# Kernel tuning notes

Measured on AMD Instinct MI355X. Metric: run time of the kernel, lower is better.

The kernel has to match this reference:

```python
import jax, jax.numpy as jnp
import numpy as np

Q_R = jnp.array([-1.0 / np.sqrt(2.0), 1.0 / np.sqrt(2.0)], dtype=jnp.float32)
N_U, N_H, N_MLP, N_CONV, N_Q = 8, 12, 16, 2, 2


def setup_inputs() -> dict:
    B, n = 16, 1024
    key = jax.random.key(0)
    ks = jax.random.split(key, 24)
    lin_w = lambda k, o, i: (jax.random.normal(k, (o, i), jnp.float32) * 0.1)
    lin_b = lambda k, o: (jax.random.normal(k, (o,), jnp.float32) * 0.1)
    inp = {
        "y": jax.random.normal(ks[0], (B, n), jnp.float32),
        "H": jax.random.normal(ks[1], (B, n, n), jnp.float32),
        "r": jax.random.normal(ks[2], (B, n), jnp.float32),
        "nu_r": jax.random.uniform(ks[3], (B, n), jnp.float32),
        "adj": (jax.random.uniform(ks[4], (B, n, n)) < 0.05).astype(jnp.float32),
        # W1: Linear(2, n_u) plus extra bias b1
        "W1_w": lin_w(ks[5], N_U, 2), "W1_b": lin_b(ks[6], N_U),
        "b1": jnp.zeros((N_U,), jnp.float32),
        # msg_mlp: Linear(3*n_u, n_mlp_hidden) -> ReLU -> Linear(n_mlp_hidden, n_u)
        "Wm1_w": lin_w(ks[7], N_MLP, 3 * N_U), "Wm1_b": lin_b(ks[8], N_MLP),
        "Wm2_w": lin_w(ks[9], N_U, N_MLP), "Wm2_b": lin_b(ks[10], N_U),
        # GRUCell(n_u + 2, n_h); gate order: r, z, n
        "gru_w_ih": lin_w(ks[11], 3 * N_H, N_U + 2), "gru_w_hh": lin_w(ks[12], 3 * N_H, N_H),
        "gru_b_ih": lin_b(ks[13], 3 * N_H), "gru_b_hh": lin_b(ks[14], 3 * N_H),
        # W2: Linear(n_h, n_u) plus extra bias b2
        "W2_w": lin_w(ks[15], N_U, N_H), "W2_b": lin_b(ks[16], N_U),
        "b2": jnp.zeros((N_U,), jnp.float32),
        # readout: Linear(n_u, n_mlp_hidden) -> ReLU -> Linear(n_mlp_hidden, N_Q)
        "Wr1_w": lin_w(ks[17], N_MLP, N_U), "Wr1_b": lin_b(ks[18], N_MLP),
        "Wr2_w": lin_w(ks[19], N_Q, N_MLP), "Wr2_b": lin_b(ks[20], N_Q),
    }
    return inp


def reference(y, H, r, nu_r, adj, W1_w, W1_b, b1, Wm1_w, Wm1_b, Wm2_w, Wm2_b,
              gru_w_ih, gru_w_hh, gru_b_ih, gru_b_hh, W2_w, W2_b, b2,
              Wr1_w, Wr1_b, Wr2_w, Wr2_b):
    B, n = y.shape
    yh = jnp.einsum('bi,bij->bj', y, H)          # (B,n)
    hh = jnp.sum(H * H, axis=1)                  # (B,n), column norms
    feat = jnp.stack([yh, hh], axis=-1)          # (B,n,2)
    u = feat @ W1_w.T + W1_b + b1                # (B,n,n_u)
    G = jnp.einsum('bki,bkj->bij', H, H)         # H^T H, (B,n,n)
    a_i = jnp.stack([r, jnp.maximum(nu_r, 1e-10)], axis=-1)  # (B,n,2)

    # masked-sum aggregation, fused (same math as expand+cat+mask+sum):
    #   agg = [u_i * deg_i, sum_j adj_ij u_j, (sum_j adj_ij G_ij) * 1_{n_u}]
    deg = jnp.sum(adj, axis=2)                   # (B,n)
    eg = jnp.sum(adj * G, axis=2)                # (B,n)
    eg_part = jnp.repeat(eg[..., None], N_U, axis=-1)  # (B,n,n_u)

    s = jnp.zeros((B, n, N_H), dtype=y.dtype)
    for _ in range(N_CONV):
        agg = jnp.concatenate([
            u * deg[..., None],
            jnp.einsum('bij,bjd->bid', adj, u),
            eg_part,
        ], axis=-1)                              # (B,n,3*n_u)
        m = jax.nn.relu(agg @ Wm1_w.T + Wm1_b) @ Wm2_w.T + Wm2_b  # (B,n,n_u)
        x = jnp.concatenate([m, a_i], axis=-1)   # (B,n,n_u+2)
        gx = x @ gru_w_ih.T + gru_b_ih
        gh = s @ gru_w_hh.T + gru_b_hh
        xr, xz, xn = jnp.split(gx, 3, axis=-1)
        hr, hz, hn = jnp.split(gh, 3, axis=-1)
        rg = jax.nn.sigmoid(xr + hr)
        zg = jax.nn.sigmoid(xz + hz)
        ng = jnp.tanh(xn + rg * hn)
        s = (1.0 - zg) * ng + zg * s             # (B,n,n_h)
        u = s @ W2_w.T + W2_b + b2               # (B,n,n_u)

    logits = jax.nn.relu(u @ Wr1_w.T + Wr1_b) @ Wr2_w.T + Wr2_b  # (B,n,N_Q)
    p = jax.nn.softmax(logits, axis=-1)
    x_hat = jnp.sum(p * Q_R, axis=-1)            # (B,n)
    nu_x = jnp.sum(p * (Q_R - x_hat[..., None]) ** 2, axis=-1)
    nu_x = jnp.maximum(nu_x, 1e-10)
    return (x_hat, nu_x)
```

## Files before the change

### kernel.cpp

```cpp
#include <hip/hip_runtime.h>

#define NB 16
#define NN 1024
#define NBN (NB * NN)
#define MAXN 128
#define NU 8
#define NH 12
#define NMLP 16
#define KC 16
#define NCHUNK (NN / KC)

#define QSW(j, c) (((j) << 4) + ((((c) ^ (((j) >> 2) & 3)) & 3) << 2))

__global__ __launch_bounds__(256) void k_build_idx(
    const float* __restrict__ adj, unsigned short* __restrict__ idxT,
    int* __restrict__ cnt, float* __restrict__ deg,
    float* __restrict__ eg, float* __restrict__ yh, float* __restrict__ hh) {
  const int row = blockIdx.x * 4 + (threadIdx.x >> 6);
  const int lane = threadIdx.x & 63;
  const float4* arow = (const float4*)(adj + (size_t)row * NN);
  float4 v[4];
#pragma unroll
  for (int rep = 0; rep < 4; ++rep) v[rep] = arow[rep * 64 + lane];
  const unsigned long long ltmask = (1ull << lane) - 1ull;
  int base = 0;
#pragma unroll
  for (int rep = 0; rep < 4; ++rep) {
    float c[4] = {v[rep].x, v[rep].y, v[rep].z, v[rep].w};
#pragma unroll
    for (int cc = 0; cc < 4; ++cc) {
      bool nz = (c[cc] != 0.0f);
      unsigned long long m = __ballot(nz);
      if (nz) {
        int p = base + __popcll(m & ltmask);
        if (p < MAXN)
          idxT[(size_t)p * NBN + row] = (unsigned short)(rep * 256 + lane * 4 + cc);
      }
      base += __popcll(m);
    }
  }
  if (lane == 0) {
    cnt[row] = base < MAXN ? base : MAXN;
    deg[row] = (float)base;
    eg[row] = 0.f; yh[row] = 0.f; hh[row] = 0.f;
  }
}

__global__ __launch_bounds__(512) void k_eg(
    const float* __restrict__ H, const float* __restrict__ y,
    const unsigned short* __restrict__ idxT, const int* __restrict__ cnt,
    float* __restrict__ eg, float* __restrict__ yh, float* __restrict__ hh) {
  __shared__ float hsT[NN * KC];
  const int b = blockIdx.x >> 6;
  const int k0 = (blockIdx.x & 63) * KC;
  const int tid = threadIdx.x;
  const float* Hb = H + ((size_t)b * NN + k0) * NN;

  for (int j0 = tid; j0 < NN; j0 += 512) {
    float hv[KC];
#pragma unroll
    for (int k = 0; k < KC; ++k) hv[k] = Hb[(size_t)k * NN + j0];
#pragma unroll
    for (int c = 0; c < 4; ++c)
      *(float4*)&hsT[QSW(j0, c)] = ((const float4*)hv)[c];
  }
  __syncthreads();

  {
    float yv[KC];
#pragma unroll
    for (int k = 0; k < KC; ++k) yv[k] = y[b * NN + k0 + k];
    for (int j = tid; j < NN; j += 512) {
      float hv[KC];
#pragma unroll
      for (int c = 0; c < 4; ++c)
        ((float4*)hv)[c] = *(const float4*)&hsT[QSW(j, c)];
      float py = 0.f, ph = 0.f;
#pragma unroll
      for (int k = 0; k < KC; ++k) { py += yv[k] * hv[k]; ph += hv[k] * hv[k]; }
      atomicAdd(&yh[b * NN + j], py);
      atomicAdd(&hh[b * NN + j], ph);
    }
  }

  for (int rep = 0; rep < 2; ++rep) {
    const int i = rep * 512 + tid;
    const int node = b * NN + i;
    const int nnz = cnt[node];
    int mx = nnz;
#pragma unroll
    for (int off = 32; off; off >>= 1) mx = max(mx, __shfl_xor(mx, off, 64));
    float hi[KC];
#pragma unroll
    for (int c = 0; c < 4; ++c)
      ((float4*)hi)[c] = *(const float4*)&hsT[QSW(i, c)];
    float acc = 0.f;
    int jcur = (nnz > 0) ? (int)idxT[node] : 0;
    for (int t = 0; t < mx; ++t) {
      int jnext = (t + 1 < nnz) ? (int)idxT[(size_t)(t + 1) * NBN + node] : 0;
      if (t < nnz) {
        float hj[KC];
#pragma unroll
        for (int c = 0; c < 4; ++c)
          ((float4*)hj)[c] = *(const float4*)&hsT[QSW(jcur, c)];
        float a0 = 0.f, a1 = 0.f, a2 = 0.f, a3 = 0.f;
#pragma unroll
        for (int k = 0; k < 4; ++k) {
          a0 += hi[k] * hj[k];
          a1 += hi[4 + k] * hj[4 + k];
          a2 += hi[8 + k] * hj[8 + k];
          a3 += hi[12 + k] * hj[12 + k];
        }
        acc += (a0 + a1) + (a2 + a3);
      }
      jcur = jnext;
    }
    atomicAdd(&eg[node], acc);
  }
}

__global__ __launch_bounds__(256) void k_u0(
    const float* __restrict__ yh, const float* __restrict__ hh,
    const float* __restrict__ W1w, const float* __restrict__ W1b,
    const float* __restrict__ b1, float* __restrict__ u) {
  const int t = blockIdx.x * 256 + threadIdx.x;
  const float a = yh[t], c = hh[t];
#pragma unroll
  for (int o = 0; o < NU; ++o)
    u[(size_t)t * NU + o] = a * W1w[2 * o] + c * W1w[2 * o + 1] + W1b[o] + b1[o];
}

__global__ __launch_bounds__(256) void k_gather(
    const float* __restrict__ u, const unsigned short* __restrict__ idxT,
    const int* __restrict__ cnt, float* __restrict__ msum) {
  const int node = blockIdx.x * 256 + threadIdx.x;
  const int nnz = cnt[node];
  int mx = nnz;
#pragma unroll
  for (int off = 32; off; off >>= 1) mx = max(mx, __shfl_xor(mx, off, 64));
  const float* ub = u + (size_t)(node & ~(NN - 1)) * NU;
  float4 acc0 = {0, 0, 0, 0}, acc1 = {0, 0, 0, 0};
  for (int t = 0; t < mx; ++t) {
    if (t < nnz) {
      int j = idxT[(size_t)t * NBN + node];
      const float4* up = (const float4*)(ub + (size_t)j * NU);
      float4 a = up[0], b4 = up[1];
      acc0.x += a.x;  acc0.y += a.y;  acc0.z += a.z;  acc0.w += a.w;
      acc1.x += b4.x; acc1.y += b4.y; acc1.z += b4.z; acc1.w += b4.w;
    }
  }
  float4* mp = (float4*)&msum[(size_t)node * NU];
  mp[0] = acc0;
  mp[1] = acc1;
}

__global__ __launch_bounds__(128) void k_update(
    const float* __restrict__ u_in, const float* __restrict__ msum,
    const float* __restrict__ deg, const float* __restrict__ eg,
    const float* __restrict__ rin, const float* __restrict__ nur,
    const float* __restrict__ Wm1w, const float* __restrict__ Wm1b,
    const float* __restrict__ Wm2w, const float* __restrict__ Wm2b,
    const float* __restrict__ gih, const float* __restrict__ ghh,
    const float* __restrict__ bih, const float* __restrict__ bhh,
    const float* __restrict__ W2w, const float* __restrict__ W2b,
    const float* __restrict__ b2,
    const float* __restrict__ Wr1w, const float* __restrict__ Wr1b,
    const float* __restrict__ Wr2w, const float* __restrict__ Wr2b,
    float* __restrict__ s, float* __restrict__ u_out, float* __restrict__ out,
    int first, int readout) {
  __shared__ float sWm1[NMLP * 3 * NU], sWm1b[NMLP], sWm2[NU * NMLP], sWm2b[NU];
  __shared__ float sgih[36 * (NU + 2)], sghh[36 * NH], sbih[36], sbhh[36];
  __shared__ float sW2[NU * NH], sW2b[NU], sb2[NU];
  __shared__ float sWr1[NMLP * NU], sWr1b[NMLP], sWr2[2 * NMLP], sWr2b[2];
  {
    auto cp = [&](float* d, const float* so, int n) {
      for (int t = threadIdx.x; t < n; t += 128) d[t] = so[t];
    };
    cp(sWm1, Wm1w, NMLP * 3 * NU); cp(sWm1b, Wm1b, NMLP);
    cp(sWm2, Wm2w, NU * NMLP);     cp(sWm2b, Wm2b, NU);
    cp(sgih, gih, 36 * (NU + 2));  cp(sghh, ghh, 36 * NH);
    cp(sbih, bih, 36);             cp(sbhh, bhh, 36);
    cp(sW2, W2w, NU * NH);         cp(sW2b, W2b, NU);   cp(sb2, b2, NU);
    cp(sWr1, Wr1w, NMLP * NU);     cp(sWr1b, Wr1b, NMLP);
    cp(sWr2, Wr2w, 2 * NMLP);      cp(sWr2b, Wr2b, 2);
  }
  __syncthreads();
  const int node = blockIdx.x * 128 + threadIdx.x;

  float agg[3 * NU];
  const float d = deg[node], e = eg[node];
#pragma unroll
  for (int o = 0; o < NU; ++o) {
    agg[o] = u_in[(size_t)node * NU + o] * d;
    agg[NU + o] = msum[(size_t)node * NU + o];
    agg[2 * NU + o] = e;
  }
  float h1[NMLP];
#pragma unroll
  for (int h = 0; h < NMLP; ++h) {
    float t = sWm1b[h];
#pragma unroll
    for (int i = 0; i < 3 * NU; ++i) t += sWm1[h * 3 * NU + i] * agg[i];
    h1[h] = fmaxf(t, 0.f);
  }
  float x[NU + 2];
#pragma unroll
  for (int o = 0; o < NU; ++o) {
    float t = sWm2b[o];
#pragma unroll
    for (int h = 0; h < NMLP; ++h) t += sWm2[o * NMLP + h] * h1[h];
    x[o] = t;
  }
  x[NU] = rin[node];
  x[NU + 1] = fmaxf(nur[node], 1e-10f);

  float sv[NH];
#pragma unroll
  for (int g = 0; g < NH; ++g) sv[g] = first ? 0.f : s[(size_t)node * NH + g];

  float sn[NH];
#pragma unroll
  for (int g = 0; g < NH; ++g) {
    float xr = sbih[g], xz = sbih[NH + g], xn = sbih[2 * NH + g];
#pragma unroll
    for (int i = 0; i < NU + 2; ++i) {
      xr += sgih[g * (NU + 2) + i] * x[i];
      xz += sgih[(NH + g) * (NU + 2) + i] * x[i];
      xn += sgih[(2 * NH + g) * (NU + 2) + i] * x[i];
    }
    float hr = sbhh[g], hz = sbhh[NH + g], hn = sbhh[2 * NH + g];
    if (!first) {
#pragma unroll
      for (int i = 0; i < NH; ++i) {
        hr += sghh[g * NH + i] * sv[i];
        hz += sghh[(NH + g) * NH + i] * sv[i];
        hn += sghh[(2 * NH + g) * NH + i] * sv[i];
      }
    }
    float rg = 1.f / (1.f + expf(-(xr + hr)));
    float zg = 1.f / (1.f + expf(-(xz + hz)));
    float ng = tanhf(xn + rg * hn);
    sn[g] = (1.f - zg) * ng + zg * sv[g];
  }
#pragma unroll
  for (int g = 0; g < NH; ++g) s[(size_t)node * NH + g] = sn[g];

  float un[NU];
#pragma unroll
  for (int o = 0; o < NU; ++o) {
    float t = sW2b[o] + sb2[o];
#pragma unroll
    for (int h = 0; h < NH; ++h) t += sW2[o * NH + h] * sn[h];
    un[o] = t;
    u_out[(size_t)node * NU + o] = t;
  }

  if (readout) {
    float h2[NMLP];
#pragma unroll
    for (int h = 0; h < NMLP; ++h) {
      float t = sWr1b[h];
#pragma unroll
      for (int o = 0; o < NU; ++o) t += sWr1[h * NU + o] * un[o];
      h2[h] = fmaxf(t, 0.f);
    }
    float l0 = sWr2b[0], l1 = sWr2b[1];
#pragma unroll
    for (int h = 0; h < NMLP; ++h) {
      l0 += sWr2[h] * h2[h];
      l1 += sWr2[NMLP + h] * h2[h];
    }
    float mx = fmaxf(l0, l1);
    float e0 = expf(l0 - mx), e1 = expf(l1 - mx);
    float inv = 1.f / (e0 + e1);
    float p0 = e0 * inv, p1 = e1 * inv;
    const float q0 = -0.70710678118654752f, q1 = 0.70710678118654752f;
    float xh = p0 * q0 + p1 * q1;
    float nu = p0 * (q0 - xh) * (q0 - xh) + p1 * (q1 - xh) * (q1 - xh);
    out[node] = xh;
    out[NB * NN + node] = fmaxf(nu, 1e-10f);
  }
}

extern "C" void kernel_launch(void* const* d_in, const int* in_sizes, int n_in,
                              void* d_out, int out_size, void* d_ws,
                              size_t ws_size, hipStream_t stream) {
  const float* y    = (const float*)d_in[0];
  const float* H    = (const float*)d_in[1];
  const float* r    = (const float*)d_in[2];
  const float* nur  = (const float*)d_in[3];
  const float* adj  = (const float*)d_in[4];
  const float* W1w  = (const float*)d_in[5];
  const float* W1b  = (const float*)d_in[6];
  const float* b1   = (const float*)d_in[7];
  const float* Wm1w = (const float*)d_in[8];
  const float* Wm1b = (const float*)d_in[9];
  const float* Wm2w = (const float*)d_in[10];
  const float* Wm2b = (const float*)d_in[11];
  const float* gih  = (const float*)d_in[12];
  const float* ghh  = (const float*)d_in[13];
  const float* bih  = (const float*)d_in[14];
  const float* bhh  = (const float*)d_in[15];
  const float* W2w  = (const float*)d_in[16];
  const float* W2b  = (const float*)d_in[17];
  const float* b2   = (const float*)d_in[18];
  const float* Wr1w = (const float*)d_in[19];
  const float* Wr1b = (const float*)d_in[20];
  const float* Wr2w = (const float*)d_in[21];
  const float* Wr2b = (const float*)d_in[22];
  float* out = (float*)d_out;

  char* p = (char*)d_ws;
  auto carve = [&](size_t bytes) {
    void* q = (void*)p;
    p += (bytes + 255) & ~(size_t)255;
    return q;
  };
  unsigned short* idxT = (unsigned short*)carve((size_t)MAXN * NBN * 2);
  int*   cnt  = (int*)  carve((size_t)NBN * 4);
  float* deg  = (float*)carve((size_t)NBN * 4);
  float* eg   = (float*)carve((size_t)NBN * 4);
  float* yh   = (float*)carve((size_t)NBN * 4);
  float* hh   = (float*)carve((size_t)NBN * 4);
  float* u    = (float*)carve((size_t)NBN * NU * 4);
  float* s    = (float*)carve((size_t)NBN * NH * 4);
  float* msum = (float*)carve((size_t)NBN * NU * 4);

  k_build_idx<<<NBN / 4, 256, 0, stream>>>(adj, idxT, cnt, deg, eg, yh, hh);
  k_eg<<<NB * NCHUNK, 512, 0, stream>>>(H, y, idxT, cnt, eg, yh, hh);
  k_u0<<<NBN / 256, 256, 0, stream>>>(yh, hh, W1w, W1b, b1, u);

  for (int it = 0; it < 2; ++it) {
    k_gather<<<NBN / 256, 256, 0, stream>>>(u, idxT, cnt, msum);
    k_update<<<NBN / 128, 128, 0, stream>>>(
        u, msum, deg, eg, r, nur, Wm1w, Wm1b, Wm2w, Wm2b, gih, ghh, bih, bhh,
        W2w, W2b, b2, Wr1w, Wr1b, Wr2w, Wr2b, s, u, out,
        it == 0, it == 1);
  }
}
```

Measured before the change: 416.3 us.

## Fuse neighbor gather into update kernel and re-swizzle H tile with float2

Merges the separate gather and update kernels into one per-iteration kernel that sums neighbor features in registers, removing the msum round trip and two launches. To avoid a read/write race on u, it ping-pongs between two u buffers. The shared-memory H tile uses a new float2-granularity XOR swizzle. The eg loop now runs to each thread's own nnz instead of the wave maximum, dropping the guard branch. The fused kernel uses 64-thread blocks, so every block reloads all the weights into shared memory, which adds per-block overhead.

```diff
diff --git a/kernel.cpp b/kernel.cpp
--- a/kernel.cpp
+++ b/kernel.cpp
@@ -10,7 +10,7 @@
 #define KC 16
 #define NCHUNK (NN / KC)
 
-#define QSW(j, c) (((j) << 4) + ((((c) ^ (((j) >> 2) & 3)) & 3) << 2))
+#define GSW(j, h) (((j) << 4) + ((((h) ^ ((j) >> 1)) & 7) << 1))
 
 __global__ __launch_bounds__(256) void k_build_idx(
     const float* __restrict__ adj, unsigned short* __restrict__ idxT,
@@ -61,8 +61,8 @@
 #pragma unroll
     for (int k = 0; k < KC; ++k) hv[k] = Hb[(size_t)k * NN + j0];
 #pragma unroll
-    for (int c = 0; c < 4; ++c)
-      *(float4*)&hsT[QSW(j0, c)] = ((const float4*)hv)[c];
+    for (int h = 0; h < 8; ++h)
+      *(float2*)&hsT[GSW(j0, h)] = make_float2(hv[2 * h], hv[2 * h + 1]);
   }
   __syncthreads();
 
@@ -71,13 +71,13 @@
 #pragma unroll
     for (int k = 0; k < KC; ++k) yv[k] = y[b * NN + k0 + k];
     for (int j = tid; j < NN; j += 512) {
-      float hv[KC];
-#pragma unroll
-      for (int c = 0; c < 4; ++c)
-        ((float4*)hv)[c] = *(const float4*)&hsT[QSW(j, c)];
       float py = 0.f, ph = 0.f;
 #pragma unroll
-      for (int k = 0; k < KC; ++k) { py += yv[k] * hv[k]; ph += hv[k] * hv[k]; }
+      for (int h = 0; h < 8; ++h) {
+        float2 hv = *(const float2*)&hsT[GSW(j, h)];
+        py += yv[2 * h] * hv.x + yv[2 * h + 1] * hv.y;
+        ph += hv.x * hv.x + hv.y * hv.y;
+      }
       atomicAdd(&yh[b * NN + j], py);
       atomicAdd(&hh[b * NN + j], ph);
     }
@@ -87,35 +87,27 @@
     const int i = rep * 512 + tid;
     const int node = b * NN + i;
     const int nnz = cnt[node];
-    int mx = nnz;
-#pragma unroll
-    for (int off = 32; off; off >>= 1) mx = max(mx, __shfl_xor(mx, off, 64));
-    float hi[KC];
-#pragma unroll
-    for (int c = 0; c < 4; ++c)
-      ((float4*)hi)[c] = *(const float4*)&hsT[QSW(i, c)];
-    float acc = 0.f;
+    float2 hi2[8];
+#pragma unroll
+    for (int h = 0; h < 8; ++h) hi2[h] = *(const float2*)&hsT[GSW(i, h)];
+    float a0 = 0.f, a1 = 0.f, a2 = 0.f, a3 = 0.f;
     int jcur = (nnz > 0) ? (int)idxT[node] : 0;
-    for (int t = 0; t < mx; ++t) {
+    for (int t = 0; t < nnz; ++t) {
       int jnext = (t + 1 < nnz) ? (int)idxT[(size_t)(t + 1) * NBN + node] : 0;
-      if (t < nnz) {
-        float hj[KC];
-#pragma unroll
-        for (int c = 0; c < 4; ++c)
-          ((float4*)hj)[c] = *(const float4*)&hsT[QSW(jcur, c)];
-        float a0 = 0.f, a1 = 0.f, a2 = 0.f, a3 = 0.f;
-#pragma unroll
-        for (int k = 0; k < 4; ++k) {
-          a0 += hi[k] * hj[k];
-          a1 += hi[4 + k] * hj[4 + k];
-          a2 += hi[8 + k] * hj[8 + k];
-          a3 += hi[12 + k] * hj[12 + k];
-        }
-        acc += (a0 + a1) + (a2 + a3);
-      }
+      float2 hj[8];
+#pragma unroll
+      for (int h = 0; h < 8; ++h) hj[h] = *(const float2*)&hsT[GSW(jcur, h)];
+      a0 += hi2[0].x * hj[0].x + hi2[0].y * hj[0].y
+          + hi2[1].x * hj[1].x + hi2[1].y * hj[1].y;
+      a1 += hi2[2].x * hj[2].x + hi2[2].y * hj[2].y
+          + hi2[3].x * hj[3].x + hi2[3].y * hj[3].y;
+      a2 += hi2[4].x * hj[4].x + hi2[4].y * hj[4].y
+          + hi2[5].x * hj[5].x + hi2[5].y * hj[5].y;
+      a3 += hi2[6].x * hj[6].x + hi2[6].y * hj[6].y
+          + hi2[7].x * hj[7].x + hi2[7].y * hj[7].y;
       jcur = jnext;
     }
-    atomicAdd(&eg[node], acc);
+    atomicAdd(&eg[node], (a0 + a1) + (a2 + a3));
   }
 }
 
@@ -130,32 +122,9 @@
     u[(size_t)t * NU + o] = a * W1w[2 * o] + c * W1w[2 * o + 1] + W1b[o] + b1[o];
 }
 
-__global__ __launch_bounds__(256) void k_gather(
-    const float* __restrict__ u, const unsigned short* __restrict__ idxT,
-    const int* __restrict__ cnt, float* __restrict__ msum) {
-  const int node = blockIdx.x * 256 + threadIdx.x;
-  const int nnz = cnt[node];
-  int mx = nnz;
-#pragma unroll
-  for (int off = 32; off; off >>= 1) mx = max(mx, __shfl_xor(mx, off, 64));
-  const float* ub = u + (size_t)(node & ~(NN - 1)) * NU;
-  float4 acc0 = {0, 0, 0, 0}, acc1 = {0, 0, 0, 0};
-  for (int t = 0; t < mx; ++t) {
-    if (t < nnz) {
-      int j = idxT[(size_t)t * NBN + node];
-      const float4* up = (const float4*)(ub + (size_t)j * NU);
-      float4 a = up[0], b4 = up[1];
-      acc0.x += a.x;  acc0.y += a.y;  acc0.z += a.z;  acc0.w += a.w;
-      acc1.x += b4.x; acc1.y += b4.y; acc1.z += b4.z; acc1.w += b4.w;
-    }
-  }
-  float4* mp = (float4*)&msum[(size_t)node * NU];
-  mp[0] = acc0;
-  mp[1] = acc1;
-}
-
-__global__ __launch_bounds__(128) void k_update(
-    const float* __restrict__ u_in, const float* __restrict__ msum,
+__global__ __launch_bounds__(64) void k_iter(
+    const float* __restrict__ u_in, const unsigned short* __restrict__ idxT,
+    const int* __restrict__ cnt,
     const float* __restrict__ deg, const float* __restrict__ eg,
     const float* __restrict__ rin, const float* __restrict__ nur,
     const float* __restrict__ Wm1w, const float* __restrict__ Wm1b,
@@ -174,7 +143,7 @@
   __shared__ float sWr1[NMLP * NU], sWr1b[NMLP], sWr2[2 * NMLP], sWr2b[2];
   {
     auto cp = [&](float* d, const float* so, int n) {
-      for (int t = threadIdx.x; t < n; t += 128) d[t] = so[t];
+      for (int t = threadIdx.x; t < n; t += 64) d[t] = so[t];
     };
     cp(sWm1, Wm1w, NMLP * 3 * NU); cp(sWm1b, Wm1b, NMLP);
     cp(sWm2, Wm2w, NU * NMLP);     cp(sWm2b, Wm2b, NU);
@@ -185,14 +154,29 @@
     cp(sWr2, Wr2w, 2 * NMLP);      cp(sWr2b, Wr2b, 2);
   }
   __syncthreads();
-  const int node = blockIdx.x * 128 + threadIdx.x;
+  const int node = blockIdx.x * 64 + threadIdx.x;
+
+  const int nnz = cnt[node];
+  const float* ub = u_in + (size_t)(node & ~(NN - 1)) * NU;
+  float4 acc0 = {0, 0, 0, 0}, acc1 = {0, 0, 0, 0};
+  int j = (nnz > 0) ? (int)idxT[node] : 0;
+  for (int t = 0; t < nnz; ++t) {
+    int jn = (t + 1 < nnz) ? (int)idxT[(size_t)(t + 1) * NBN + node] : 0;
+    const float4* up = (const float4*)(ub + (size_t)j * NU);
+    float4 a = up[0], c4 = up[1];
+    acc0.x += a.x;  acc0.y += a.y;  acc0.z += a.z;  acc0.w += a.w;
+    acc1.x += c4.x; acc1.y += c4.y; acc1.z += c4.z; acc1.w += c4.w;
+    j = jn;
+  }
+  const float msv[NU] = {acc0.x, acc0.y, acc0.z, acc0.w,
+                         acc1.x, acc1.y, acc1.z, acc1.w};
 
   float agg[3 * NU];
   const float d = deg[node], e = eg[node];
 #pragma unroll
   for (int o = 0; o < NU; ++o) {
     agg[o] = u_in[(size_t)node * NU + o] * d;
-    agg[NU + o] = msum[(size_t)node * NU + o];
+    agg[NU + o] = msv[o];
     agg[2 * NU + o] = e;
   }
   float h1[NMLP];
@@ -322,19 +306,20 @@
   float* eg   = (float*)carve((size_t)NBN * 4);
   float* yh   = (float*)carve((size_t)NBN * 4);
   float* hh   = (float*)carve((size_t)NBN * 4);
-  float* u    = (float*)carve((size_t)NBN * NU * 4);
+  float* ua   = (float*)carve((size_t)NBN * NU * 4);
+  float* ub   = (float*)carve((size_t)NBN * NU * 4);
   float* s    = (float*)carve((size_t)NBN * NH * 4);
-  float* msum = (float*)carve((size_t)NBN * NU * 4);
 
   k_build_idx<<<NBN / 4, 256, 0, stream>>>(adj, idxT, cnt, deg, eg, yh, hh);
   k_eg<<<NB * NCHUNK, 512, 0, stream>>>(H, y, idxT, cnt, eg, yh, hh);
-  k_u0<<<NBN / 256, 256, 0, stream>>>(yh, hh, W1w, W1b, b1, u);
-
-  for (int it = 0; it < 2; ++it) {
-    k_gather<<<NBN / 256, 256, 0, stream>>>(u, idxT, cnt, msum);
-    k_update<<<NBN / 128, 128, 0, stream>>>(
-        u, msum, deg, eg, r, nur, Wm1w, Wm1b, Wm2w, Wm2b, gih, ghh, bih, bhh,
-        W2w, W2b, b2, Wr1w, Wr1b, Wr2w, Wr2b, s, u, out,
-        it == 0, it == 1);
-  }
-}
+  k_u0<<<NBN / 256, 256, 0, stream>>>(yh, hh, W1w, W1b, b1, ua);
+
+  k_iter<<<NBN / 64, 64, 0, stream>>>(
+      ua, idxT, cnt, deg, eg, r, nur, Wm1w, Wm1b, Wm2w, Wm2b, gih, ghh, bih,
+      bhh, W2w, W2b, b2, Wr1w, Wr1b, Wr2w, Wr2b, s, ub, out,
+      1, 0);
+  k_iter<<<NBN / 64, 64, 0, stream>>>(
+      ub, idxT, cnt, deg, eg, r, nur, Wm1w, Wm1b, Wm2w, Wm2b, gih, ghh, bih,
+      bhh, W2w, W2b, b2, Wr1w, Wr1b, Wr2w, Wr2b, s, ua, out,
+      0, 1);
+}
```

Measured after the change: 433.8 us. 1.04x slower.

## Fuse gather, u0 and GRU update into per-phase kernels; gather raw features in phase one

Applied to the files above, without the earlier changes.

Removes the separate u0 and gather kernels and the msum buffer. Each GRU iteration becomes one templated kernel that gathers its neighbour sum inline. Phase one exploits linearity: it sums the 2-wide (yh, hh) features of neighbours and applies W1 afterwards, so it never materialises u0. The eg loop drops its wave-max bound and manual prefetch in favour of a plain per-thread loop, and yh/hh are interleaved into one float2 buffer. This cuts launches and global traffic, at the cost of smaller 64-thread blocks and divergent per-thread loop lengths.

```diff
diff --git a/kernel.cpp b/kernel.cpp
--- a/kernel.cpp
+++ b/kernel.cpp
@@ -15,7 +15,7 @@
 __global__ __launch_bounds__(256) void k_build_idx(
     const float* __restrict__ adj, unsigned short* __restrict__ idxT,
     int* __restrict__ cnt, float* __restrict__ deg,
-    float* __restrict__ eg, float* __restrict__ yh, float* __restrict__ hh) {
+    float* __restrict__ eg, float* __restrict__ yhh) {
   const int row = blockIdx.x * 4 + (threadIdx.x >> 6);
   const int lane = threadIdx.x & 63;
   const float4* arow = (const float4*)(adj + (size_t)row * NN);
@@ -42,14 +42,14 @@
   if (lane == 0) {
     cnt[row] = base < MAXN ? base : MAXN;
     deg[row] = (float)base;
-    eg[row] = 0.f; yh[row] = 0.f; hh[row] = 0.f;
+    eg[row] = 0.f; yhh[2 * row] = 0.f; yhh[2 * row + 1] = 0.f;
   }
 }
 
 __global__ __launch_bounds__(512) void k_eg(
     const float* __restrict__ H, const float* __restrict__ y,
     const unsigned short* __restrict__ idxT, const int* __restrict__ cnt,
-    float* __restrict__ eg, float* __restrict__ yh, float* __restrict__ hh) {
+    float* __restrict__ eg, float* __restrict__ yhh) {
   __shared__ float hsT[NN * KC];
   const int b = blockIdx.x >> 6;
   const int k0 = (blockIdx.x & 63) * KC;
@@ -78,8 +78,8 @@
       float py = 0.f, ph = 0.f;
 #pragma unroll
       for (int k = 0; k < KC; ++k) { py += yv[k] * hv[k]; ph += hv[k] * hv[k]; }
-      atomicAdd(&yh[b * NN + j], py);
-      atomicAdd(&hh[b * NN + j], ph);
+      atomicAdd(&yhh[(b * NN + j) * 2], py);
+      atomicAdd(&yhh[(b * NN + j) * 2 + 1], ph);
     }
   }
 
@@ -87,77 +87,38 @@
     const int i = rep * 512 + tid;
     const int node = b * NN + i;
     const int nnz = cnt[node];
-    int mx = nnz;
-#pragma unroll
-    for (int off = 32; off; off >>= 1) mx = max(mx, __shfl_xor(mx, off, 64));
     float hi[KC];
 #pragma unroll
     for (int c = 0; c < 4; ++c)
       ((float4*)hi)[c] = *(const float4*)&hsT[QSW(i, c)];
-    float acc = 0.f;
-    int jcur = (nnz > 0) ? (int)idxT[node] : 0;
-    for (int t = 0; t < mx; ++t) {
-      int jnext = (t + 1 < nnz) ? (int)idxT[(size_t)(t + 1) * NBN + node] : 0;
-      if (t < nnz) {
-        float hj[KC];
-#pragma unroll
-        for (int c = 0; c < 4; ++c)
-          ((float4*)hj)[c] = *(const float4*)&hsT[QSW(jcur, c)];
-        float a0 = 0.f, a1 = 0.f, a2 = 0.f, a3 = 0.f;
-#pragma unroll
-        for (int k = 0; k < 4; ++k) {
-          a0 += hi[k] * hj[k];
-          a1 += hi[4 + k] * hj[4 + k];
-          a2 += hi[8 + k] * hj[8 + k];
-          a3 += hi[12 + k] * hj[12 + k];
-        }
-        acc += (a0 + a1) + (a2 + a3);
+    float a0 = 0.f, a1 = 0.f, a2 = 0.f, a3 = 0.f;
+#pragma unroll 2
+    for (int t = 0; t < nnz; ++t) {
+      const int j = (int)idxT[(size_t)t * NBN + node];
+      float hj[KC];
+#pragma unroll
+      for (int c = 0; c < 4; ++c)
+        ((float4*)hj)[c] = *(const float4*)&hsT[QSW(j, c)];
+#pragma unroll
+      for (int k = 0; k < 4; ++k) {
+        a0 += hi[k] * hj[k];
+        a1 += hi[4 + k] * hj[4 + k];
+        a2 += hi[8 + k] * hj[8 + k];
+        a3 += hi[12 + k] * hj[12 + k];
       }
-      jcur = jnext;
-    }
-    atomicAdd(&eg[node], acc);
+    }
+    atomicAdd(&eg[node], (a0 + a1) + (a2 + a3));
   }
 }
 
-__global__ __launch_bounds__(256) void k_u0(
-    const float* __restrict__ yh, const float* __restrict__ hh,
-    const float* __restrict__ W1w, const float* __restrict__ W1b,
-    const float* __restrict__ b1, float* __restrict__ u) {
-  const int t = blockIdx.x * 256 + threadIdx.x;
-  const float a = yh[t], c = hh[t];
-#pragma unroll
-  for (int o = 0; o < NU; ++o)
-    u[(size_t)t * NU + o] = a * W1w[2 * o] + c * W1w[2 * o + 1] + W1b[o] + b1[o];
-}
-
-__global__ __launch_bounds__(256) void k_gather(
-    const float* __restrict__ u, const unsigned short* __restrict__ idxT,
-    const int* __restrict__ cnt, float* __restrict__ msum) {
-  const int node = blockIdx.x * 256 + threadIdx.x;
-  const int nnz = cnt[node];
-  int mx = nnz;
-#pragma unroll
-  for (int off = 32; off; off >>= 1) mx = max(mx, __shfl_xor(mx, off, 64));
-  const float* ub = u + (size_t)(node & ~(NN - 1)) * NU;
-  float4 acc0 = {0, 0, 0, 0}, acc1 = {0, 0, 0, 0};
-  for (int t = 0; t < mx; ++t) {
-    if (t < nnz) {
-      int j = idxT[(size_t)t * NBN + node];
-      const float4* up = (const float4*)(ub + (size_t)j * NU);
-      float4 a = up[0], b4 = up[1];
-      acc0.x += a.x;  acc0.y += a.y;  acc0.z += a.z;  acc0.w += a.w;
-      acc1.x += b4.x; acc1.y += b4.y; acc1.z += b4.z; acc1.w += b4.w;
-    }
-  }
-  float4* mp = (float4*)&msum[(size_t)node * NU];
-  mp[0] = acc0;
-  mp[1] = acc1;
-}
-
-__global__ __launch_bounds__(128) void k_update(
-    const float* __restrict__ u_in, const float* __restrict__ msum,
+template <int PHASE>
+__global__ __launch_bounds__(64) void k_iter(
+    const float* __restrict__ u_in, const float2* __restrict__ yhh,
+    const unsigned short* __restrict__ idxT, const int* __restrict__ cnt,
     const float* __restrict__ deg, const float* __restrict__ eg,
     const float* __restrict__ rin, const float* __restrict__ nur,
+    const float* __restrict__ W1w, const float* __restrict__ W1b,
+    const float* __restrict__ b1,
     const float* __restrict__ Wm1w, const float* __restrict__ Wm1b,
     const float* __restrict__ Wm2w, const float* __restrict__ Wm2b,
     const float* __restrict__ gih, const float* __restrict__ ghh,
@@ -166,33 +127,75 @@
     const float* __restrict__ b2,
     const float* __restrict__ Wr1w, const float* __restrict__ Wr1b,
     const float* __restrict__ Wr2w, const float* __restrict__ Wr2b,
-    float* __restrict__ s, float* __restrict__ u_out, float* __restrict__ out,
-    int first, int readout) {
+    float* __restrict__ s, float* __restrict__ u_out, float* __restrict__ out) {
   __shared__ float sWm1[NMLP * 3 * NU], sWm1b[NMLP], sWm2[NU * NMLP], sWm2b[NU];
   __shared__ float sgih[36 * (NU + 2)], sghh[36 * NH], sbih[36], sbhh[36];
   __shared__ float sW2[NU * NH], sW2b[NU], sb2[NU];
   __shared__ float sWr1[NMLP * NU], sWr1b[NMLP], sWr2[2 * NMLP], sWr2b[2];
+  __shared__ float sW1[2 * NU], sWb1[NU];
   {
     auto cp = [&](float* d, const float* so, int n) {
-      for (int t = threadIdx.x; t < n; t += 128) d[t] = so[t];
+      for (int t = threadIdx.x; t < n; t += 64) d[t] = so[t];
     };
     cp(sWm1, Wm1w, NMLP * 3 * NU); cp(sWm1b, Wm1b, NMLP);
     cp(sWm2, Wm2w, NU * NMLP);     cp(sWm2b, Wm2b, NU);
-    cp(sgih, gih, 36 * (NU + 2));  cp(sghh, ghh, 36 * NH);
+    cp(sgih, gih, 36 * (NU + 2));
     cp(sbih, bih, 36);             cp(sbhh, bhh, 36);
     cp(sW2, W2w, NU * NH);         cp(sW2b, W2b, NU);   cp(sb2, b2, NU);
-    cp(sWr1, Wr1w, NMLP * NU);     cp(sWr1b, Wr1b, NMLP);
-    cp(sWr2, Wr2w, 2 * NMLP);      cp(sWr2b, Wr2b, 2);
+    if (PHASE == 1) {
+      cp(sW1, W1w, 2 * NU);
+      for (int t = threadIdx.x; t < NU; t += 64) sWb1[t] = W1b[t] + b1[t];
+    } else {
+      cp(sghh, ghh, 36 * NH);
+      cp(sWr1, Wr1w, NMLP * NU);   cp(sWr1b, Wr1b, NMLP);
+      cp(sWr2, Wr2w, 2 * NMLP);    cp(sWr2b, Wr2b, 2);
+    }
   }
   __syncthreads();
-  const int node = blockIdx.x * 128 + threadIdx.x;
+  const int node = blockIdx.x * 64 + threadIdx.x;
+  const int nnz = cnt[node];
+  const int bbase = node & ~(NN - 1);
+
+  float uself[NU], msv[NU];
+  if (PHASE == 1) {
+    float sy = 0.f, sh = 0.f;
+#pragma unroll 4
+    for (int t = 0; t < nnz; ++t) {
+      const int j = (int)idxT[(size_t)t * NBN + node];
+      float2 v = yhh[bbase + j];
+      sy += v.x; sh += v.y;
+    }
+    const float2 w0 = yhh[node];
+    const float fn = (float)nnz;
+#pragma unroll
+    for (int o = 0; o < NU; ++o) {
+      uself[o] = w0.x * sW1[2 * o] + w0.y * sW1[2 * o + 1] + sWb1[o];
+      msv[o] = sy * sW1[2 * o] + sh * sW1[2 * o + 1] + fn * sWb1[o];
+    }
+  } else {
+    float4 acc0 = {0, 0, 0, 0}, acc1 = {0, 0, 0, 0};
+#pragma unroll 4
+    for (int t = 0; t < nnz; ++t) {
+      const int j = (int)idxT[(size_t)t * NBN + node];
+      const float4* up = (const float4*)(u_in + ((size_t)bbase + j) * NU);
+      float4 a = up[0], c4 = up[1];
+      acc0.x += a.x;  acc0.y += a.y;  acc0.z += a.z;  acc0.w += a.w;
+      acc1.x += c4.x; acc1.y += c4.y; acc1.z += c4.z; acc1.w += c4.w;
+    }
+    msv[0] = acc0.x; msv[1] = acc0.y; msv[2] = acc0.z; msv[3] = acc0.w;
+    msv[4] = acc1.x; msv[5] = acc1.y; msv[6] = acc1.z; msv[7] = acc1.w;
+    const float4* up = (const float4*)(u_in + (size_t)node * NU);
+    float4 a = up[0], c4 = up[1];
+    uself[0] = a.x;  uself[1] = a.y;  uself[2] = a.z;  uself[3] = a.w;
+    uself[4] = c4.x; uself[5] = c4.y; uself[6] = c4.z; uself[7] = c4.w;
+  }
 
   float agg[3 * NU];
   const float d = deg[node], e = eg[node];
 #pragma unroll
   for (int o = 0; o < NU; ++o) {
-    agg[o] = u_in[(size_t)node * NU + o] * d;
-    agg[NU + o] = msum[(size_t)node * NU + o];
+    agg[o] = uself[o] * d;
+    agg[NU + o] = msv[o];
     agg[2 * NU + o] = e;
   }
   float h1[NMLP];
@@ -216,7 +219,8 @@
 
   float sv[NH];
 #pragma unroll
-  for (int g = 0; g < NH; ++g) sv[g] = first ? 0.f : s[(size_t)node * NH + g];
+  for (int g = 0; g < NH; ++g)
+    sv[g] = (PHASE == 1) ? 0.f : s[(size_t)node * NH + g];
 
   float sn[NH];
 #pragma unroll
@@ -229,7 +233,7 @@
       xn += sgih[(2 * NH + g) * (NU + 2) + i] * x[i];
     }
     float hr = sbhh[g], hz = sbhh[NH + g], hn = sbhh[2 * NH + g];
-    if (!first) {
+    if (PHASE != 1) {
 #pragma unroll
       for (int i = 0; i < NH; ++i) {
         hr += sghh[g * NH + i] * sv[i];
@@ -242,8 +246,11 @@
     float ng = tanhf(xn + rg * hn);
     sn[g] = (1.f - zg) * ng + zg * sv[g];
   }
-#pragma unroll
-  for (int g = 0; g < NH; ++g) s[(size_t)node * NH + g] = sn[g];
+
+  if (PHASE == 1) {
+#pragma unroll
+    for (int g = 0; g < NH; ++g) s[(size_t)node * NH + g] = sn[g];
+  }
 
   float un[NU];
 #pragma unroll
@@ -252,10 +259,13 @@
 #pragma unroll
     for (int h = 0; h < NH; ++h) t += sW2[o * NH + h] * sn[h];
     un[o] = t;
-    u_out[(size_t)node * NU + o] = t;
-  }
-
-  if (readout) {
+  }
+  if (PHASE == 1) {
+#pragma unroll
+    for (int o = 0; o < NU; ++o) u_out[(size_t)node * NU + o] = un[o];
+  }
+
+  if (PHASE == 2) {
     float h2[NMLP];
 #pragma unroll
     for (int h = 0; h < NMLP; ++h) {
@@ -320,21 +330,19 @@
   int*   cnt  = (int*)  carve((size_t)NBN * 4);
   float* deg  = (float*)carve((size_t)NBN * 4);
   float* eg   = (float*)carve((size_t)NBN * 4);
-  float* yh   = (float*)carve((size_t)NBN * 4);
-  float* hh   = (float*)carve((size_t)NBN * 4);
+  float* yhh  = (float*)carve((size_t)NBN * 8);
   float* u    = (float*)carve((size_t)NBN * NU * 4);
   float* s    = (float*)carve((size_t)NBN * NH * 4);
-  float* msum = (float*)carve((size_t)NBN * NU * 4);
-
-  k_build_idx<<<NBN / 4, 256, 0, stream>>>(adj, idxT, cnt, deg, eg, yh, hh);
-  k_eg<<<NB * NCHUNK, 512, 0, stream>>>(H, y, idxT, cnt, eg, yh, hh);
-  k_u0<<<NBN / 256, 256, 0, stream>>>(yh, hh, W1w, W1b, b1, u);
-
-  for (int it = 0; it < 2; ++it) {
-    k_gather<<<NBN / 256, 256, 0, stream>>>(u, idxT, cnt, msum);
-    k_update<<<NBN / 128, 128, 0, stream>>>(
-        u, msum, deg, eg, r, nur, Wm1w, Wm1b, Wm2w, Wm2b, gih, ghh, bih, bhh,
-        W2w, W2b, b2, Wr1w, Wr1b, Wr2w, Wr2b, s, u, out,
-        it == 0, it == 1);
-  }
+
+  k_build_idx<<<NBN / 4, 256, 0, stream>>>(adj, idxT, cnt, deg, eg, yhh);
+  k_eg<<<NB * NCHUNK, 512, 0, stream>>>(H, y, idxT, cnt, eg, yhh);
+
+  k_iter<1><<<NBN / 64, 64, 0, stream>>>(
+      u, (const float2*)yhh, idxT, cnt, deg, eg, r, nur, W1w, W1b, b1,
+      Wm1w, Wm1b, Wm2w, Wm2b, gih, ghh, bih, bhh, W2w, W2b, b2,
+      Wr1w, Wr1b, Wr2w, Wr2b, s, u, out);
+  k_iter<2><<<NBN / 64, 64, 0, stream>>>(
+      u, (const float2*)yhh, idxT, cnt, deg, eg, r, nur, W1w, W1b, b1,
+      Wm1w, Wm1b, Wm2w, Wm2b, gih, ghh, bih, bhh, W2w, W2b, b2,
+      Wr1w, Wr1b, Wr2w, Wr2b, s, u, out);
 }
```

Result: faster. 348.1 us (-16.4%).
